# Kernel optimization log

Hardware: AMD Instinct MI355X
Metric: run time of the kernel (lower is better)

## Reference

```python
import jax, jax.numpy as jnp
import numpy as np

B, L, T, IN, H, OUT = 1024, 64, 128, 13, 64, 13
NEG = -1e30


def gru_step(x, h, Wih, Whh, bih, bhh):
    # PyTorch GRU cell: gates ordered (r, z, n)
    gi = x @ Wih.T + bih          # [B, 3H]
    gh = h @ Whh.T + bhh          # [B, 3H]
    ir, iz, inn = jnp.split(gi, 3, axis=-1)
    hr, hz, hn = jnp.split(gh, 3, axis=-1)
    r = jax.nn.sigmoid(ir + hr)
    z = jax.nn.sigmoid(iz + hz)
    n = jnp.tanh(inn + r * hn)
    return (1.0 - z) * n + z * h


def setup_inputs() -> dict:
    key = jax.random.key(0)
    ks = jax.random.split(key, 10)
    s = float(1.0 / np.sqrt(H))
    x = jax.random.normal(ks[0], (B, L, IN), jnp.float32)
    lengths = jax.random.randint(ks[1], (B,), 1, L + 1).at[0].set(L)
    Wih = jax.random.uniform(ks[2], (3 * H, IN), jnp.float32, -s, s)
    Whh = jax.random.uniform(ks[3], (3 * H, H), jnp.float32, -s, s)
    bih = jax.random.uniform(ks[4], (3 * H,), jnp.float32, -s, s)
    bhh = jax.random.uniform(ks[5], (3 * H,), jnp.float32, -s, s)
    Wf = jax.random.uniform(ks[6], (OUT, H), jnp.float32, -s, s)
    bf = jax.random.uniform(ks[7], (OUT,), jnp.float32, -s, s)
    Wa = jax.random.uniform(ks[8], (H, H), jnp.float32, -s, s)
    ba = jax.random.uniform(ks[9], (H,), jnp.float32, -s, s)
    return dict(x=x, lengths=lengths, output_length=T, Wih=Wih, Whh=Whh,
                bih=bih, bhh=bhh, Wf=Wf, bf=bf, Wa=Wa, ba=ba)


def reference(x, lengths, output_length, Wih, Whh, bih, bhh, Wf, bf, Wa, ba):
    b, l = x.shape[0], x.shape[1]
    xT = jnp.swapaxes(x, 0, 1)                        # [L, B, IN]
    h0 = jnp.zeros((b, H), x.dtype)

    # Encoder: masked GRU emulating pack_padded/pad_packed semantics:
    # hidden frozen past each sequence's length; outputs zero past length.
    def enc(h, inp):
        t, xt = inp
        hn = gru_step(xt, h, Wih, Whh, bih, bhh)
        valid = (t < lengths)[:, None]
        h = jnp.where(valid, hn, h)
        return h, jnp.where(valid, hn, 0.0)

    h, outs = jax.lax.scan(enc, h0, (jnp.arange(l), xT))
    # output[:, -1, :] of the padded output (zeros for seqs shorter than max)
    nin = outs[-1] @ Wf.T + bf                        # [B, OUT]

    Tn = output_length
    buf0 = jnp.zeros((Tn, b, H), x.dtype)             # growing past-prediction buffer

    def dec(carry, t):
        h, buf, nin = carry
        hn = gru_step(nin, h, Wih, Whh, bih, bhh)     # output_lstm == hidden (1 layer, 1 step)
        # attention recomputed over all past predictions (softmax over time axis)
        logits = jnp.einsum('tbh,gh->tbg', buf, Wa) + ba      # [T, B, H]
        logits = jnp.where((jnp.arange(Tn) < t)[:, None, None], logits, NEG)
        w = jax.nn.softmax(logits, axis=0)
        o = hn + jnp.sum(w * buf, axis=0)             # at t=0 buffer is all zeros -> +0
        y = o @ Wf.T + bf
        return (hn, buf.at[t].set(o), y), y

    _, ys = jax.lax.scan(dec, (h, buf0, nin), jnp.arange(Tn))
    return jnp.swapaxes(ys, 0, 1)                     # [B, T, OUT]
```

## Files before the change

kernel.cpp:

```cpp
#include <hip/hip_runtime.h>
#include <stdint.h>
#include <math.h>

#define BATCH 1024
#define SEQL  64
#define TDEC  128
#define NIN   13
#define NH    64
#define NOUT  13

typedef _Float16 h2 __attribute__((ext_vector_type(2)));
typedef __fp16   g2 __attribute__((ext_vector_type(2)));

union FU  { uint32_t u; float f; };
union HU  { uint16_t u; _Float16 h; };
union H2U { uint32_t u; h2 h; g2 g; };

__device__ __forceinline__ float bf2f(uint16_t v) { FU t; t.u = ((uint32_t)v) << 16; return t.f; }
__device__ __forceinline__ float hf2f(uint16_t v) { HU t; t.u = v; return (float)t.h; }

__device__ __forceinline__ float ldf(const void* p, long i, int mode) {
    if (mode == 1) return bf2f(((const uint16_t*)p)[i]);
    if (mode == 2) return hf2f(((const uint16_t*)p)[i]);
    return ((const float*)p)[i];
}

__device__ __forceinline__ bool pass_stats(const void* p, int n, int lane, int mode,
                                           float band_lo, float band_hi, float max_ok) {
    int m = (n + 1) / 2;
    int cnt = (m < 64) ? m : 64;
    bool ok_max = true, in_band = false;
    if (lane < cnt) {
        long pos = 2L * (((long)lane * m) / cnt);
        float v = (mode == 1) ? bf2f(((const uint16_t*)p)[pos])
                              : hf2f(((const uint16_t*)p)[pos]);
        float a = fabsf(v);
        ok_max  = (a <= max_ok);
        in_band = (a >= band_lo && a <= band_hi);
    }
    bool allmax = __all(ok_max);
    int nb = (int)__popcll(__ballot(in_band));
    int need = cnt / 4; if (need < 1) need = 1;
    return allmax && (nb >= need);
}
__device__ __forceinline__ int detect(const void* p, int n, int lane,
                                      float band_lo, float band_hi, float max_ok) {
    if (pass_stats(p, n, lane, 1, band_lo, band_hi, max_ok)) return 1;
    if (pass_stats(p, n, lane, 2, band_lo, band_hi, max_ok)) return 2;
    return 0;
}
__device__ __forceinline__ bool detect_len64(const int* p, int lane) {
    int v = p[2 * lane + 1];
    return __all(v == 0);
}

__device__ __forceinline__ float dot2(h2 a, h2 b, float c) {
#if __has_builtin(__builtin_amdgcn_fdot2)
    return __builtin_amdgcn_fdot2(a, b, c, false);
#else
    return c + (float)a[0] * (float)b[0] + (float)a[1] * (float)b[1];
#endif
}
__device__ __forceinline__ uint32_t pku(float a, float b) {
    H2U t; t.g = __builtin_amdgcn_cvt_pkrtz(a, b); return t.u;
}
__device__ __forceinline__ h2 uh(uint32_t u) { H2U t; t.u = u; return t.h; }
__device__ __forceinline__ float rcp_(float x) { return __builtin_amdgcn_rcpf(x); }
__device__ __forceinline__ float sigm(float x)  { return rcp_(1.0f + __expf(-x)); }
__device__ __forceinline__ float tanh_(float x) { return 1.0f - 2.0f * rcp_(__expf(2.0f * x) + 1.0f); }
__device__ __forceinline__ void wb() { __builtin_amdgcn_wave_barrier(); }

__device__ __forceinline__ float swap1(float v) {
    FU a; a.f = v;
    FU b; b.u = (uint32_t)__builtin_amdgcn_mov_dpp((int)a.u, 0xB1, 0xF, 0xF, true);
    return b.f;
}

#define BCAST32(vreg, dst)                                                 \
    {                                                                      \
        uint32_t _pr = pku((vreg), swap1(vreg));                           \
        _Pragma("unroll")                                                  \
        for (int _k = 0; _k < 32; ++_k)                                    \
            (dst)[_k] = __builtin_amdgcn_readlane(_pr, 2 * _k);            \
    }

__global__ __launch_bounds__(64, 1)
void gru_attn_kernel(const void* __restrict__ x, const int* __restrict__ lengths,
                     const void* __restrict__ Wih, const void* __restrict__ Whh,
                     const void* __restrict__ bih, const void* __restrict__ bhh,
                     const void* __restrict__ Wf, const void* __restrict__ bfv,
                     const void* __restrict__ Wa, const void* __restrict__ ba,
                     float* __restrict__ out)
{
    const int b = blockIdx.x;
    const int j = threadIdx.x;

    __shared__ __align__(16) uint32_t xs2[SEQL][8];

    const int dX   = detect(x,   BATCH * SEQL * NIN, j, 0.25f, 4.0f, 16.0f);
    const int dWih = detect(Wih, 3 * NH * NIN, j, 0.04f, 0.13f, 0.14f);
    const int dWhh = detect(Whh, 3 * NH * NH,  j, 0.04f, 0.13f, 0.14f);
    const int dBih = detect(bih, 3 * NH,       j, 0.04f, 0.13f, 0.14f);
    const int dBhh = detect(bhh, 3 * NH,       j, 0.04f, 0.13f, 0.14f);
    const int dWf  = detect(Wf,  NOUT * NH,    j, 0.04f, 0.13f, 0.14f);
    const int dBf  = detect(bfv, NOUT,         j, 0.04f, 0.13f, 0.14f);
    const int dWa  = detect(Wa,  NH * NH,      j, 0.04f, 0.13f, 0.14f);
    const int dBa  = detect(ba,  NH,           j, 0.04f, 0.13f, 0.14f);
    const bool len64 = detect_len64(lengths, j);

    h2 wihr[7], wihz[7], wihn[7];
    h2 whhr[32], whhz[32], whhn[32];
    h2 wap[32], wfp[32];

#pragma unroll
    for (int k = 0; k < 7; ++k) {
        float a0 = ldf(Wih, (0 * NH + j) * NIN + 2 * k, dWih);
        float a1 = (2 * k + 1 < NIN) ? ldf(Wih, (0 * NH + j) * NIN + 2 * k + 1, dWih) : 0.0f;
        wihr[k] = uh(pku(a0, a1));
        float b0 = ldf(Wih, (1 * NH + j) * NIN + 2 * k, dWih);
        float b1 = (2 * k + 1 < NIN) ? ldf(Wih, (1 * NH + j) * NIN + 2 * k + 1, dWih) : 0.0f;
        wihz[k] = uh(pku(b0, b1));
        float c0 = ldf(Wih, (2 * NH + j) * NIN + 2 * k, dWih);
        float c1 = (2 * k + 1 < NIN) ? ldf(Wih, (2 * NH + j) * NIN + 2 * k + 1, dWih) : 0.0f;
        wihn[k] = uh(pku(c0, c1));
    }
    const int jf = (j < NOUT) ? j : 0;
#pragma unroll
    for (int k = 0; k < 32; ++k) {
        whhr[k] = uh(pku(ldf(Whh, (0 * NH + j) * NH + 2 * k, dWhh),
                         ldf(Whh, (0 * NH + j) * NH + 2 * k + 1, dWhh)));
        whhz[k] = uh(pku(ldf(Whh, (1 * NH + j) * NH + 2 * k, dWhh),
                         ldf(Whh, (1 * NH + j) * NH + 2 * k + 1, dWhh)));
        whhn[k] = uh(pku(ldf(Whh, (2 * NH + j) * NH + 2 * k, dWhh),
                         ldf(Whh, (2 * NH + j) * NH + 2 * k + 1, dWhh)));
        wap[k]  = uh(pku(ldf(Wa, j * NH + 2 * k, dWa),
                         ldf(Wa, j * NH + 2 * k + 1, dWa)));
        wfp[k]  = uh(pku(ldf(Wf, jf * NH + 2 * k, dWf),
                         ldf(Wf, jf * NH + 2 * k + 1, dWf)));
    }

    const float bcr = ldf(bih, j, dBih)          + ldf(bhh, j, dBhh);
    const float bcz = ldf(bih, NH + j, dBih)     + ldf(bhh, NH + j, dBhh);
    const float bni = ldf(bih, 2 * NH + j, dBih);
    const float bnh = ldf(bhh, 2 * NH + j, dBhh);
    const float baj = ldf(ba, j, dBa);
    const float bfj = ldf(bfv, jf, dBf);
    const int len = len64 ? lengths[2 * b] : lengths[b];

    {
        const long base = ((long)b * SEQL + j) * NIN;
        float v[14];
#pragma unroll
        for (int k = 0; k < NIN; ++k) v[k] = ldf(x, base + k, dX);
        v[13] = 0.0f;
#pragma unroll
        for (int p = 0; p < 7; ++p) xs2[j][p] = pku(v[2 * p], v[2 * p + 1]);
        xs2[j][7] = 0u;
    }
    wb();

    float h = 0.0f;
    float out_last = 0.0f;

    uint32_t hpk[32];
    BCAST32(h, hpk);

#pragma unroll 1
    for (int t = 0; t < SEQL; ++t) {
        uint4 q0 = *(const uint4*)xs2[t];
        uint4 q1 = *(const uint4*)(xs2[t] + 4);

        float arA = bcr, azA = bcz, hnA = bnh, anA = bni;
        float arB = 0.0f, azB = 0.0f, hnB = 0.0f;
        float arC = 0.0f, azC = 0.0f, hnC = 0.0f;
        float arD = 0.0f, azD = 0.0f, hnD = 0.0f;
#pragma unroll
        for (int k = 0; k < 32; k += 4) {
            h2 h0 = uh(hpk[k]), h1 = uh(hpk[k + 1]), h2v = uh(hpk[k + 2]), h3 = uh(hpk[k + 3]);
            arA = dot2(whhr[k],     h0, arA); azA = dot2(whhz[k],     h0, azA); hnA = dot2(whhn[k],     h0, hnA);
            arB = dot2(whhr[k + 1], h1, arB); azB = dot2(whhz[k + 1], h1, azB); hnB = dot2(whhn[k + 1], h1, hnB);
            arC = dot2(whhr[k + 2], h2v, arC); azC = dot2(whhz[k + 2], h2v, azC); hnC = dot2(whhn[k + 2], h2v, hnC);
            arD = dot2(whhr[k + 3], h3, arD); azD = dot2(whhz[k + 3], h3, azD); hnD = dot2(whhn[k + 3], h3, hnD);
        }
        {
            uint32_t xw[8] = {q0.x, q0.y, q0.z, q0.w, q1.x, q1.y, q1.z, q1.w};
#pragma unroll
            for (int p = 0; p < 7; ++p) {
                h2 xv = uh(xw[p]);
                arB = dot2(wihr[p], xv, arB);
                azB = dot2(wihz[p], xv, azB);
                anA = dot2(wihn[p], xv, anA);
            }
        }
        float ar = (arA + arB) + (arC + arD);
        float az = (azA + azB) + (azC + azD);
        float hna = (hnA + hnB) + (hnC + hnD);
        float r = sigm(ar);
        float z = sigm(az);
        float n = tanh_(anA + r * hna);
        float hnew = n + z * (h - n);
        if (t < len) h = hnew;
        if (t == SEQL - 1) out_last = (t < len) ? hnew : 0.0f;
        BCAST32(h, hpk);
    }

    uint32_t ypk[7];
    {
        uint32_t opk[32];
        BCAST32(out_last, opk);
        float nA = bfj, nB = 0.0f, nC = 0.0f, nD = 0.0f;
#pragma unroll
        for (int k = 0; k < 32; k += 4) {
            nA = dot2(wfp[k],     uh(opk[k]),     nA);
            nB = dot2(wfp[k + 1], uh(opk[k + 1]), nB);
            nC = dot2(wfp[k + 2], uh(opk[k + 2]), nC);
            nD = dot2(wfp[k + 3], uh(opk[k + 3]), nD);
        }
        float nv = (nA + nB) + (nC + nD);
        float nz = (j < NOUT) ? nv : 0.0f;
        uint32_t pr = pku(nz, swap1(nz));
#pragma unroll
        for (int k = 0; k < 7; ++k) ypk[k] = __builtin_amdgcn_readlane(pr, 2 * k);
    }

    float m = -1e30f, Zs = 0.0f, num = 0.0f;

#pragma unroll 1
    for (int t = 0; t < TDEC; ++t) {
        float arA = bcr, azA = bcz, hnA = bnh, anA = bni;
        float arB = 0.0f, azB = 0.0f, hnB = 0.0f;
        float arC = 0.0f, azC = 0.0f, hnC = 0.0f;
        float arD = 0.0f, azD = 0.0f, hnD = 0.0f;
#pragma unroll
        for (int k = 0; k < 32; k += 4) {
            h2 h0 = uh(hpk[k]), h1 = uh(hpk[k + 1]), h2v = uh(hpk[k + 2]), h3 = uh(hpk[k + 3]);
            arA = dot2(whhr[k],     h0, arA); azA = dot2(whhz[k],     h0, azA); hnA = dot2(whhn[k],     h0, hnA);
            arB = dot2(whhr[k + 1], h1, arB); azB = dot2(whhz[k + 1], h1, azB); hnB = dot2(whhn[k + 1], h1, hnB);
            arC = dot2(whhr[k + 2], h2v, arC); azC = dot2(whhz[k + 2], h2v, azC); hnC = dot2(whhn[k + 2], h2v, hnC);
            arD = dot2(whhr[k + 3], h3, arD); azD = dot2(whhz[k + 3], h3, azD); hnD = dot2(whhn[k + 3], h3, hnD);
        }
#pragma unroll
        for (int p = 0; p < 7; ++p) {
            h2 xv = uh(ypk[p]);
            arB = dot2(wihr[p], xv, arB);
            azB = dot2(wihz[p], xv, azB);
            anA = dot2(wihn[p], xv, anA);
        }
        float ar = (arA + arB) + (arC + arD);
        float az = (azA + azB) + (azC + azD);
        float hna = (hnA + hnB) + (hnC + hnD);
        float r = sigm(ar);
        float z = sigm(az);
        float n = tanh_(anA + r * hna);
        float hnew = n + z * (h - n);
        h = hnew;
        float attn = (t > 0) ? num * rcp_(Zs) : 0.0f;
        float o = hnew + attn;

        BCAST32(hnew, hpk);
        uint32_t opk[32];
        BCAST32(o, opk);

        float sA = baj, yA = bfj, sB = 0.0f, yB = 0.0f, sC = 0.0f, yC = 0.0f, sD = 0.0f, yD = 0.0f;
#pragma unroll
        for (int k = 0; k < 32; k += 4) {
            h2 o0 = uh(opk[k]), o1 = uh(opk[k + 1]), o2 = uh(opk[k + 2]), o3 = uh(opk[k + 3]);
            sA = dot2(wap[k],     o0, sA); yA = dot2(wfp[k],     o0, yA);
            sB = dot2(wap[k + 1], o1, sB); yB = dot2(wfp[k + 1], o1, yB);
            sC = dot2(wap[k + 2], o2, sC); yC = dot2(wfp[k + 2], o2, yC);
            sD = dot2(wap[k + 3], o3, sD); yD = dot2(wfp[k + 3], o3, yD);
        }
        float s  = (sA + sB) + (sC + sD);
        float yv = (yA + yB) + (yC + yD);
        float mn = fmaxf(m, s);
        float al = __expf(m - mn);
        float p  = __expf(s - mn);
        Zs  = Zs * al + p;
        num = num * al + p * o;
        m = mn;
        if (j < NOUT) out[((size_t)b * TDEC + t) * NOUT + j] = yv;
        float yz = (j < NOUT) ? yv : 0.0f;
        uint32_t pr = pku(yz, swap1(yz));
#pragma unroll
        for (int k = 0; k < 7; ++k) ypk[k] = __builtin_amdgcn_readlane(pr, 2 * k);
    }
}

extern "C" void kernel_launch(void* const* d_in, const int* in_sizes, int n_in,
                              void* d_out, int out_size, void* d_ws, size_t ws_size,
                              hipStream_t stream) {
    (void)in_sizes; (void)n_in; (void)out_size; (void)d_ws; (void)ws_size;
    const void* x      = d_in[0];
    const int* lengths = (const int*)d_in[1];
    const void* Wih = d_in[3];
    const void* Whh = d_in[4];
    const void* bih = d_in[5];
    const void* bhh = d_in[6];
    const void* Wf  = d_in[7];
    const void* bf  = d_in[8];
    const void* Wa  = d_in[9];
    const void* ba  = d_in[10];
    float* out = (float*)d_out;

    gru_attn_kernel<<<dim3(BATCH), dim3(64), 0, stream>>>(
        x, lengths, Wih, Whh, bih, bhh, Wf, bf, Wa, ba, out);
}
```

Measured before the change: 224.3 us.

## Batch 16 sequences per wave and compute GRU and attention with MFMA

```diff
diff --git a/kernel.cpp b/kernel.cpp
--- a/kernel.cpp
+++ b/kernel.cpp
@@ -8,13 +8,17 @@
 #define NIN   13
 #define NH    64
 #define NOUT  13
-
-typedef _Float16 h2 __attribute__((ext_vector_type(2)));
-typedef __fp16   g2 __attribute__((ext_vector_type(2)));
+#define NB    16
+
+typedef float    f32x4 __attribute__((ext_vector_type(4)));
+typedef _Float16 f16x8 __attribute__((ext_vector_type(8)));
+typedef _Float16 h2    __attribute__((ext_vector_type(2)));
+typedef __fp16   g2    __attribute__((ext_vector_type(2)));
 
 union FU  { uint32_t u; float f; };
 union HU  { uint16_t u; _Float16 h; };
 union H2U { uint32_t u; h2 h; g2 g; };
+union FRG { uint32_t u[4]; f16x8 v; };
 
 __device__ __forceinline__ float bf2f(uint16_t v) { FU t; t.u = ((uint32_t)v) << 16; return t.f; }
 __device__ __forceinline__ float hf2f(uint16_t v) { HU t; t.u = v; return (float)t.h; }
@@ -54,34 +58,93 @@
     return __all(v == 0);
 }
 
-__device__ __forceinline__ float dot2(h2 a, h2 b, float c) {
-#if __has_builtin(__builtin_amdgcn_fdot2)
-    return __builtin_amdgcn_fdot2(a, b, c, false);
-#else
-    return c + (float)a[0] * (float)b[0] + (float)a[1] * (float)b[1];
-#endif
-}
 __device__ __forceinline__ uint32_t pku(float a, float b) {
     H2U t; t.g = __builtin_amdgcn_cvt_pkrtz(a, b); return t.u;
 }
-__device__ __forceinline__ h2 uh(uint32_t u) { H2U t; t.u = u; return t.h; }
 __device__ __forceinline__ float rcp_(float x) { return __builtin_amdgcn_rcpf(x); }
-__device__ __forceinline__ float sigm(float x)  { return rcp_(1.0f + __expf(-x)); }
-__device__ __forceinline__ float tanh_(float x) { return 1.0f - 2.0f * rcp_(__expf(2.0f * x) + 1.0f); }
-__device__ __forceinline__ void wb() { __builtin_amdgcn_wave_barrier(); }
-
-__device__ __forceinline__ float swap1(float v) {
-    FU a; a.f = v;
-    FU b; b.u = (uint32_t)__builtin_amdgcn_mov_dpp((int)a.u, 0xB1, 0xF, 0xF, true);
-    return b.f;
-}
-
-#define BCAST32(vreg, dst)                                                 \
+__device__ __forceinline__ float exp2_(float x) {
+#if __has_builtin(__builtin_amdgcn_exp2f)
+    return __builtin_amdgcn_exp2f(x);
+#else
+    return __expf(x * 0.69314718056f);
+#endif
+}
+__device__ __forceinline__ float sigm2(float xs)  { return rcp_(1.0f + exp2_(-xs)); }
+__device__ __forceinline__ float tanh2(float xs)  { return 1.0f - 2.0f * rcp_(exp2_(xs) + 1.0f); }
+
+#define MFMA(A, B, C) __builtin_amdgcn_mfma_f32_16x16x32_f16((A), (B), (C), 0, 0, 0)
+
+
+__device__ __forceinline__ f16x8 afrag_w(const void* W, int dt, int row, int stride,
+                                         int kbase, int g, float scale) {
+    float v[8];
+#pragma unroll
+    for (int jj = 0; jj < 4; ++jj)
+        v[jj] = ldf(W, (long)row * stride + kbase + 4 * g + jj, dt) * scale;
+#pragma unroll
+    for (int jj = 0; jj < 4; ++jj)
+        v[4 + jj] = ldf(W, (long)row * stride + kbase + 16 + 4 * g + jj, dt) * scale;
+    FRG t;
+    t.u[0] = pku(v[0], v[1]); t.u[1] = pku(v[2], v[3]);
+    t.u[2] = pku(v[4], v[5]); t.u[3] = pku(v[6], v[7]);
+    return t.v;
+}
+__device__ __forceinline__ f16x8 afrag_ih(const void* W, int dt, int row, int g,
+                                          float bias, float scale) {
+    float v[4];
+#pragma unroll
+    for (int jj = 0; jj < 4; ++jj) {
+        int k = 4 * g + jj;
+        v[jj] = (k < NIN) ? ldf(W, (long)row * NIN + k, dt) * scale
+                          : ((k == NIN) ? bias * scale : 0.0f);
+    }
+    FRG t;
+    t.u[0] = pku(v[0], v[1]); t.u[1] = pku(v[2], v[3]);
+    t.u[2] = 0u; t.u[3] = 0u;
+    return t.v;
+}
+__device__ __forceinline__ f16x8 afrag_wf(const void* W, int dt, int row16,
+                                          int kbase, int g) {
+    float v[8];
+#pragma unroll
+    for (int jj = 0; jj < 4; ++jj)
+        v[jj] = (row16 < NOUT) ? ldf(W, (long)row16 * NH + kbase + 4 * g + jj, dt) : 0.0f;
+#pragma unroll
+    for (int jj = 0; jj < 4; ++jj)
+        v[4 + jj] = (row16 < NOUT) ? ldf(W, (long)row16 * NH + kbase + 16 + 4 * g + jj, dt) : 0.0f;
+    FRG t;
+    t.u[0] = pku(v[0], v[1]); t.u[1] = pku(v[2], v[3]);
+    t.u[2] = pku(v[4], v[5]); t.u[3] = pku(v[6], v[7]);
+    return t.v;
+}
+
+#define PACKB(S, F0, F1)                                                   \
+    { FRG _a, _b;                                                          \
+      _a.u[0] = pku(S[0][0], S[0][1]); _a.u[1] = pku(S[0][2], S[0][3]);    \
+      _a.u[2] = pku(S[1][0], S[1][1]); _a.u[3] = pku(S[1][2], S[1][3]);    \
+      _b.u[0] = pku(S[2][0], S[2][1]); _b.u[1] = pku(S[2][2], S[2][3]);    \
+      _b.u[2] = pku(S[3][0], S[3][1]); _b.u[3] = pku(S[3][2], S[3][3]);    \
+      (F0) = _a.v; (F1) = _b.v; }
+
+#define GATES(BF)                                                          \
+    f32x4 dR[4], dZ[4], dNh[4], dNi[4];                                    \
     {                                                                      \
-        uint32_t _pr = pku((vreg), swap1(vreg));                           \
-        _Pragma("unroll")                                                  \
-        for (int _k = 0; _k < 32; ++_k)                                    \
-            (dst)[_k] = __builtin_amdgcn_readlane(_pr, 2 * _k);            \
+        f32x4 zz = {0.0f, 0.0f, 0.0f, 0.0f};                               \
+        _Pragma("unroll") for (int mt = 0; mt < 4; ++mt) {                 \
+            dR[mt]  = MFMA(Ar[mt][0], hbF0, zz);                           \
+            dZ[mt]  = MFMA(Az[mt][0], hbF0, zz);                           \
+            dNh[mt] = MFMA(An[mt][0], hbF0, zz);                           \
+        }                                                                  \
+        _Pragma("unroll") for (int mt = 0; mt < 4; ++mt) {                 \
+            dR[mt]  = MFMA(Ar[mt][1], hbF1, dR[mt]);                       \
+            dZ[mt]  = MFMA(Az[mt][1], hbF1, dZ[mt]);                       \
+            dNh[mt] = MFMA(An[mt][1], hbF1, dNh[mt]);                      \
+        }                                                                  \
+        _Pragma("unroll") for (int mt = 0; mt < 4; ++mt) {                 \
+            dR[mt]  = MFMA(Air[mt], BF, dR[mt]);                           \
+            dZ[mt]  = MFMA(Aiz[mt], BF, dZ[mt]);                           \
+            dNi[mt] = MFMA(Ain[mt], BF, zz);                               \
+        }                                                                  \
     }
 
 __global__ __launch_bounds__(64, 1)
@@ -92,197 +155,210 @@
                      const void* __restrict__ Wa, const void* __restrict__ ba,
                      float* __restrict__ out)
 {
-    const int b = blockIdx.x;
-    const int j = threadIdx.x;
-
-    __shared__ __align__(16) uint32_t xs2[SEQL][8];
-
-    const int dX   = detect(x,   BATCH * SEQL * NIN, j, 0.25f, 4.0f, 16.0f);
-    const int dWih = detect(Wih, 3 * NH * NIN, j, 0.04f, 0.13f, 0.14f);
-    const int dWhh = detect(Whh, 3 * NH * NH,  j, 0.04f, 0.13f, 0.14f);
-    const int dBih = detect(bih, 3 * NH,       j, 0.04f, 0.13f, 0.14f);
-    const int dBhh = detect(bhh, 3 * NH,       j, 0.04f, 0.13f, 0.14f);
-    const int dWf  = detect(Wf,  NOUT * NH,    j, 0.04f, 0.13f, 0.14f);
-    const int dBf  = detect(bfv, NOUT,         j, 0.04f, 0.13f, 0.14f);
-    const int dWa  = detect(Wa,  NH * NH,      j, 0.04f, 0.13f, 0.14f);
-    const int dBa  = detect(ba,  NH,           j, 0.04f, 0.13f, 0.14f);
-    const bool len64 = detect_len64(lengths, j);
-
-    h2 wihr[7], wihz[7], wihn[7];
-    h2 whhr[32], whhz[32], whhn[32];
-    h2 wap[32], wfp[32];
-
-#pragma unroll
-    for (int k = 0; k < 7; ++k) {
-        float a0 = ldf(Wih, (0 * NH + j) * NIN + 2 * k, dWih);
-        float a1 = (2 * k + 1 < NIN) ? ldf(Wih, (0 * NH + j) * NIN + 2 * k + 1, dWih) : 0.0f;
-        wihr[k] = uh(pku(a0, a1));
-        float b0 = ldf(Wih, (1 * NH + j) * NIN + 2 * k, dWih);
-        float b1 = (2 * k + 1 < NIN) ? ldf(Wih, (1 * NH + j) * NIN + 2 * k + 1, dWih) : 0.0f;
-        wihz[k] = uh(pku(b0, b1));
-        float c0 = ldf(Wih, (2 * NH + j) * NIN + 2 * k, dWih);
-        float c1 = (2 * k + 1 < NIN) ? ldf(Wih, (2 * NH + j) * NIN + 2 * k + 1, dWih) : 0.0f;
-        wihn[k] = uh(pku(c0, c1));
-    }
-    const int jf = (j < NOUT) ? j : 0;
-#pragma unroll
-    for (int k = 0; k < 32; ++k) {
-        whhr[k] = uh(pku(ldf(Whh, (0 * NH + j) * NH + 2 * k, dWhh),
-                         ldf(Whh, (0 * NH + j) * NH + 2 * k + 1, dWhh)));
-        whhz[k] = uh(pku(ldf(Whh, (1 * NH + j) * NH + 2 * k, dWhh),
-                         ldf(Whh, (1 * NH + j) * NH + 2 * k + 1, dWhh)));
-        whhn[k] = uh(pku(ldf(Whh, (2 * NH + j) * NH + 2 * k, dWhh),
-                         ldf(Whh, (2 * NH + j) * NH + 2 * k + 1, dWhh)));
-        wap[k]  = uh(pku(ldf(Wa, j * NH + 2 * k, dWa),
-                         ldf(Wa, j * NH + 2 * k + 1, dWa)));
-        wfp[k]  = uh(pku(ldf(Wf, jf * NH + 2 * k, dWf),
-                         ldf(Wf, jf * NH + 2 * k + 1, dWf)));
-    }
-
-    const float bcr = ldf(bih, j, dBih)          + ldf(bhh, j, dBhh);
-    const float bcz = ldf(bih, NH + j, dBih)     + ldf(bhh, NH + j, dBhh);
-    const float bni = ldf(bih, 2 * NH + j, dBih);
-    const float bnh = ldf(bhh, 2 * NH + j, dBhh);
-    const float baj = ldf(ba, j, dBa);
-    const float bfj = ldf(bfv, jf, dBf);
-    const int len = len64 ? lengths[2 * b] : lengths[b];
-
+    const int l  = threadIdx.x;
+    const int g  = l >> 4;
+    const int c  = l & 15;
+    const int b0 = blockIdx.x * NB;
+
+    const int dX   = detect(x,   BATCH * SEQL * NIN, l, 0.25f, 4.0f, 16.0f);
+    const int dWih = detect(Wih, 3 * NH * NIN, l, 0.04f, 0.13f, 0.14f);
+    const int dWhh = detect(Whh, 3 * NH * NH,  l, 0.04f, 0.13f, 0.14f);
+    const int dBih = detect(bih, 3 * NH,       l, 0.04f, 0.13f, 0.14f);
+    const int dBhh = detect(bhh, 3 * NH,       l, 0.04f, 0.13f, 0.14f);
+    const int dWf  = detect(Wf,  NOUT * NH,    l, 0.04f, 0.13f, 0.14f);
+    const int dBf  = detect(bfv, NOUT,         l, 0.04f, 0.13f, 0.14f);
+    const int dWa  = detect(Wa,  NH * NH,      l, 0.04f, 0.13f, 0.14f);
+    const int dBa  = detect(ba,  NH,           l, 0.04f, 0.13f, 0.14f);
+    const bool len64 = detect_len64(lengths, l);
+
+    const float L2E  = 1.44269504089f;
+    const float L2E2 = 2.88539008177f;
+
+    f16x8 Ar[4][2], Az[4][2], An[4][2];
+    f16x8 Air[4], Aiz[4], Ain[4];
+    f16x8 Awa[4][2], Awf[2];
+
+#pragma unroll
+    for (int mt = 0; mt < 4; ++mt) {
+#pragma unroll
+        for (int kc = 0; kc < 2; ++kc) {
+            Ar[mt][kc] = afrag_w(Whh, dWhh,       mt * 16 + c, NH, kc * 32, g, L2E);
+            Az[mt][kc] = afrag_w(Whh, dWhh,  64 + mt * 16 + c, NH, kc * 32, g, L2E);
+            An[mt][kc] = afrag_w(Whh, dWhh, 128 + mt * 16 + c, NH, kc * 32, g, L2E2);
+            Awa[mt][kc] = afrag_w(Wa, dWa,        mt * 16 + c, NH, kc * 32, g, L2E);
+        }
+        int rr = mt * 16 + c;
+        float br = ldf(bih, rr, dBih)            + ldf(bhh, rr, dBhh);
+        float bz = ldf(bih, NH + rr, dBih)       + ldf(bhh, NH + rr, dBhh);
+        float bn = ldf(bih, 2 * NH + rr, dBih);
+        Air[mt] = afrag_ih(Wih, dWih,            rr, g, br, L2E);
+        Aiz[mt] = afrag_ih(Wih, dWih,  64 + rr,     g, bz, L2E);
+        Ain[mt] = afrag_ih(Wih, dWih, 128 + rr,     g, bn, L2E2);
+    }
+#pragma unroll
+    for (int kc = 0; kc < 2; ++kc) Awf[kc] = afrag_wf(Wf, dWf, c, kc * 32, g);
+
+    float bnhS[4][4], bajS[4][4], bfS[4];
+#pragma unroll
+    for (int mt = 0; mt < 4; ++mt)
+#pragma unroll
+        for (int reg = 0; reg < 4; ++reg) {
+            int row = mt * 16 + 4 * g + reg;
+            bnhS[mt][reg] = ldf(bhh, 2 * NH + row, dBhh) * L2E2;
+            bajS[mt][reg] = ldf(ba, row, dBa) * L2E;
+        }
+#pragma unroll
+    for (int reg = 0; reg < 4; ++reg) {
+        int row = 4 * g + reg;
+        bfS[reg] = (row < NOUT) ? ldf(bfv, row, dBf) : 0.0f;
+    }
+
+    const int lenc = len64 ? lengths[2 * (b0 + c)] : lengths[b0 + c];
+
+    float hc[4][4];
+    float ol[4][4];
+#pragma unroll
+    for (int mt = 0; mt < 4; ++mt)
+#pragma unroll
+        for (int reg = 0; reg < 4; ++reg) { hc[mt][reg] = 0.0f; ol[mt][reg] = 0.0f; }
+    f16x8 hbF0, hbF1;
+    { FRG zf; zf.u[0] = zf.u[1] = zf.u[2] = zf.u[3] = 0u; hbF0 = zf.v; hbF1 = zf.v; }
+
+    float xpre[4];
     {
-        const long base = ((long)b * SEQL + j) * NIN;
-        float v[14];
-#pragma unroll
-        for (int k = 0; k < NIN; ++k) v[k] = ldf(x, base + k, dX);
-        v[13] = 0.0f;
-#pragma unroll
-        for (int p = 0; p < 7; ++p) xs2[j][p] = pku(v[2 * p], v[2 * p + 1]);
-        xs2[j][7] = 0u;
-    }
-    wb();
-
-    float h = 0.0f;
-    float out_last = 0.0f;
-
-    uint32_t hpk[32];
-    BCAST32(h, hpk);
+        const long base = ((long)(b0 + c) * SEQL + 0) * NIN;
+#pragma unroll
+        for (int jj = 0; jj < 4; ++jj) {
+            int k = 4 * g + jj;
+            xpre[jj] = (k < NIN) ? ldf(x, base + k, dX) : ((k == NIN) ? 1.0f : 0.0f);
+        }
+    }
 
 #pragma unroll 1
     for (int t = 0; t < SEQL; ++t) {
-        uint4 q0 = *(const uint4*)xs2[t];
-        uint4 q1 = *(const uint4*)(xs2[t] + 4);
-
-        float arA = bcr, azA = bcz, hnA = bnh, anA = bni;
-        float arB = 0.0f, azB = 0.0f, hnB = 0.0f;
-        float arC = 0.0f, azC = 0.0f, hnC = 0.0f;
-        float arD = 0.0f, azD = 0.0f, hnD = 0.0f;
-#pragma unroll
-        for (int k = 0; k < 32; k += 4) {
-            h2 h0 = uh(hpk[k]), h1 = uh(hpk[k + 1]), h2v = uh(hpk[k + 2]), h3 = uh(hpk[k + 3]);
-            arA = dot2(whhr[k],     h0, arA); azA = dot2(whhz[k],     h0, azA); hnA = dot2(whhn[k],     h0, hnA);
-            arB = dot2(whhr[k + 1], h1, arB); azB = dot2(whhz[k + 1], h1, azB); hnB = dot2(whhn[k + 1], h1, hnB);
-            arC = dot2(whhr[k + 2], h2v, arC); azC = dot2(whhz[k + 2], h2v, azC); hnC = dot2(whhn[k + 2], h2v, hnC);
-            arD = dot2(whhr[k + 3], h3, arD); azD = dot2(whhz[k + 3], h3, azD); hnD = dot2(whhn[k + 3], h3, hnD);
-        }
+        FRG xb;
+        xb.u[0] = pku(xpre[0], xpre[1]);
+        xb.u[1] = pku(xpre[2], xpre[3]);
+        xb.u[2] = 0u; xb.u[3] = 0u;
+        f16x8 xbF = xb.v;
         {
-            uint32_t xw[8] = {q0.x, q0.y, q0.z, q0.w, q1.x, q1.y, q1.z, q1.w};
-#pragma unroll
-            for (int p = 0; p < 7; ++p) {
-                h2 xv = uh(xw[p]);
-                arB = dot2(wihr[p], xv, arB);
-                azB = dot2(wihz[p], xv, azB);
-                anA = dot2(wihn[p], xv, anA);
-            }
-        }
-        float ar = (arA + arB) + (arC + arD);
-        float az = (azA + azB) + (azC + azD);
-        float hna = (hnA + hnB) + (hnC + hnD);
-        float r = sigm(ar);
-        float z = sigm(az);
-        float n = tanh_(anA + r * hna);
-        float hnew = n + z * (h - n);
-        if (t < len) h = hnew;
-        if (t == SEQL - 1) out_last = (t < len) ? hnew : 0.0f;
-        BCAST32(h, hpk);
-    }
-
-    uint32_t ypk[7];
+            int tt = (t + 1 < SEQL) ? t + 1 : t;
+            const long base = ((long)(b0 + c) * SEQL + tt) * NIN;
+#pragma unroll
+            for (int jj = 0; jj < 4; ++jj) {
+                int k = 4 * g + jj;
+                xpre[jj] = (k < NIN) ? ldf(x, base + k, dX) : ((k == NIN) ? 1.0f : 0.0f);
+            }
+        }
+
+        GATES(xbF)
+
+#pragma unroll
+        for (int mt = 0; mt < 4; ++mt)
+#pragma unroll
+            for (int reg = 0; reg < 4; ++reg) {
+                float rr = sigm2(dR[mt][reg]);
+                float zv = sigm2(dZ[mt][reg]);
+                float nn = tanh2(dNi[mt][reg] + rr * (dNh[mt][reg] + bnhS[mt][reg]));
+                float hn = nn + zv * (hc[mt][reg] - nn);
+                bool upd = (t < lenc);
+                if (t == SEQL - 1) ol[mt][reg] = upd ? hn : 0.0f;
+                hc[mt][reg] = upd ? hn : hc[mt][reg];
+            }
+        PACKB(hc, hbF0, hbF1)
+    }
+
+    f16x8 ybF;
     {
-        uint32_t opk[32];
-        BCAST32(out_last, opk);
-        float nA = bfj, nB = 0.0f, nC = 0.0f, nD = 0.0f;
-#pragma unroll
-        for (int k = 0; k < 32; k += 4) {
-            nA = dot2(wfp[k],     uh(opk[k]),     nA);
-            nB = dot2(wfp[k + 1], uh(opk[k + 1]), nB);
-            nC = dot2(wfp[k + 2], uh(opk[k + 2]), nC);
-            nD = dot2(wfp[k + 3], uh(opk[k + 3]), nD);
-        }
-        float nv = (nA + nB) + (nC + nD);
-        float nz = (j < NOUT) ? nv : 0.0f;
-        uint32_t pr = pku(nz, swap1(nz));
-#pragma unroll
-        for (int k = 0; k < 7; ++k) ypk[k] = __builtin_amdgcn_readlane(pr, 2 * k);
-    }
-
-    float m = -1e30f, Zs = 0.0f, num = 0.0f;
+        f16x8 obF0, obF1;
+        PACKB(ol, obF0, obF1)
+        f32x4 zz = {0.0f, 0.0f, 0.0f, 0.0f};
+        f32x4 dY = MFMA(Awf[0], obF0, zz);
+        dY = MFMA(Awf[1], obF1, dY);
+        float yv[4];
+#pragma unroll
+        for (int reg = 0; reg < 4; ++reg) yv[reg] = dY[reg] + bfS[reg];
+        float y1 = (g == 3) ? 1.0f : yv[1];
+        FRG yb;
+        yb.u[0] = pku(yv[0], y1);
+        yb.u[1] = pku(yv[2], yv[3]);
+        yb.u[2] = 0u; yb.u[3] = 0u;
+        ybF = yb.v;
+    }
+
+    float mS[4][4], ZS[4][4], numS[4][4];
+#pragma unroll
+    for (int mt = 0; mt < 4; ++mt)
+#pragma unroll
+        for (int reg = 0; reg < 4; ++reg) {
+            mS[mt][reg] = -1e30f; ZS[mt][reg] = 0.0f; numS[mt][reg] = 0.0f;
+        }
 
 #pragma unroll 1
     for (int t = 0; t < TDEC; ++t) {
-        float arA = bcr, azA = bcz, hnA = bnh, anA = bni;
-        float arB = 0.0f, azB = 0.0f, hnB = 0.0f;
-        float arC = 0.0f, azC = 0.0f, hnC = 0.0f;
-        float arD = 0.0f, azD = 0.0f, hnD = 0.0f;
-#pragma unroll
-        for (int k = 0; k < 32; k += 4) {
-            h2 h0 = uh(hpk[k]), h1 = uh(hpk[k + 1]), h2v = uh(hpk[k + 2]), h3 = uh(hpk[k + 3]);
-            arA = dot2(whhr[k],     h0, arA); azA = dot2(whhz[k],     h0, azA); hnA = dot2(whhn[k],     h0, hnA);
-            arB = dot2(whhr[k + 1], h1, arB); azB = dot2(whhz[k + 1], h1, azB); hnB = dot2(whhn[k + 1], h1, hnB);
-            arC = dot2(whhr[k + 2], h2v, arC); azC = dot2(whhz[k + 2], h2v, azC); hnC = dot2(whhn[k + 2], h2v, hnC);
-            arD = dot2(whhr[k + 3], h3, arD); azD = dot2(whhz[k + 3], h3, azD); hnD = dot2(whhn[k + 3], h3, hnD);
-        }
-#pragma unroll
-        for (int p = 0; p < 7; ++p) {
-            h2 xv = uh(ypk[p]);
-            arB = dot2(wihr[p], xv, arB);
-            azB = dot2(wihz[p], xv, azB);
-            anA = dot2(wihn[p], xv, anA);
-        }
-        float ar = (arA + arB) + (arC + arD);
-        float az = (azA + azB) + (azC + azD);
-        float hna = (hnA + hnB) + (hnC + hnD);
-        float r = sigm(ar);
-        float z = sigm(az);
-        float n = tanh_(anA + r * hna);
-        float hnew = n + z * (h - n);
-        h = hnew;
-        float attn = (t > 0) ? num * rcp_(Zs) : 0.0f;
-        float o = hnew + attn;
-
-        BCAST32(hnew, hpk);
-        uint32_t opk[32];
-        BCAST32(o, opk);
-
-        float sA = baj, yA = bfj, sB = 0.0f, yB = 0.0f, sC = 0.0f, yC = 0.0f, sD = 0.0f, yD = 0.0f;
-#pragma unroll
-        for (int k = 0; k < 32; k += 4) {
-            h2 o0 = uh(opk[k]), o1 = uh(opk[k + 1]), o2 = uh(opk[k + 2]), o3 = uh(opk[k + 3]);
-            sA = dot2(wap[k],     o0, sA); yA = dot2(wfp[k],     o0, yA);
-            sB = dot2(wap[k + 1], o1, sB); yB = dot2(wfp[k + 1], o1, yB);
-            sC = dot2(wap[k + 2], o2, sC); yC = dot2(wfp[k + 2], o2, yC);
-            sD = dot2(wap[k + 3], o3, sD); yD = dot2(wfp[k + 3], o3, yD);
-        }
-        float s  = (sA + sB) + (sC + sD);
-        float yv = (yA + yB) + (yC + yD);
-        float mn = fmaxf(m, s);
-        float al = __expf(m - mn);
-        float p  = __expf(s - mn);
-        Zs  = Zs * al + p;
-        num = num * al + p * o;
-        m = mn;
-        if (j < NOUT) out[((size_t)b * TDEC + t) * NOUT + j] = yv;
-        float yz = (j < NOUT) ? yv : 0.0f;
-        uint32_t pr = pku(yz, swap1(yz));
-#pragma unroll
-        for (int k = 0; k < 7; ++k) ypk[k] = __builtin_amdgcn_readlane(pr, 2 * k);
+        GATES(ybF)
+
+#pragma unroll
+        for (int mt = 0; mt < 4; ++mt)
+#pragma unroll
+            for (int reg = 0; reg < 4; ++reg) {
+                float rr = sigm2(dR[mt][reg]);
+                float zv = sigm2(dZ[mt][reg]);
+                float nn = tanh2(dNi[mt][reg] + rr * (dNh[mt][reg] + bnhS[mt][reg]));
+                hc[mt][reg] = nn + zv * (hc[mt][reg] - nn);
+            }
+        PACKB(hc, hbF0, hbF1)
+
+        float oc[4][4];
+#pragma unroll
+        for (int mt = 0; mt < 4; ++mt)
+#pragma unroll
+            for (int reg = 0; reg < 4; ++reg) {
+                float a_ = numS[mt][reg] * rcp_(ZS[mt][reg]);
+                oc[mt][reg] = hc[mt][reg] + ((t > 0) ? a_ : 0.0f);
+            }
+        f16x8 obF0, obF1;
+        PACKB(oc, obF0, obF1)
+
+        f32x4 dS[4], dY;
+        {
+            f32x4 zz = {0.0f, 0.0f, 0.0f, 0.0f};
+#pragma unroll
+            for (int mt = 0; mt < 4; ++mt) dS[mt] = MFMA(Awa[mt][0], obF0, zz);
+#pragma unroll
+            for (int mt = 0; mt < 4; ++mt) dS[mt] = MFMA(Awa[mt][1], obF1, dS[mt]);
+            dY = MFMA(Awf[0], obF0, zz);
+            dY = MFMA(Awf[1], obF1, dY);
+        }
+
+#pragma unroll
+        for (int mt = 0; mt < 4; ++mt)
+#pragma unroll
+            for (int reg = 0; reg < 4; ++reg) {
+                float s_ = dS[mt][reg] + bajS[mt][reg];
+                float mn = fmaxf(mS[mt][reg], s_);
+                float al = exp2_(mS[mt][reg] - mn);
+                float pp = exp2_(s_ - mn);
+                ZS[mt][reg]  = ZS[mt][reg] * al + pp;
+                numS[mt][reg] = numS[mt][reg] * al + pp * oc[mt][reg];
+                mS[mt][reg] = mn;
+            }
+
+        float yv[4];
+#pragma unroll
+        for (int reg = 0; reg < 4; ++reg) yv[reg] = dY[reg] + bfS[reg];
+#pragma unroll
+        for (int reg = 0; reg < 4; ++reg) {
+            int row = 4 * g + reg;
+            if (row < NOUT)
+                out[((size_t)(b0 + c) * TDEC + t) * NOUT + row] = yv[reg];
+        }
+        float y1 = (g == 3) ? 1.0f : yv[1];
+        FRG yb;
+        yb.u[0] = pku(yv[0], y1);
+        yb.u[1] = pku(yv[2], yv[3]);
+        yb.u[2] = 0u; yb.u[3] = 0u;
+        ybF = yb.v;
     }
 }
 
@@ -302,6 +378,6 @@
     const void* ba  = d_in[10];
     float* out = (float*)d_out;
 
-    gru_attn_kernel<<<dim3(BATCH), dim3(64), 0, stream>>>(
+    gru_attn_kernel<<<dim3(BATCH / NB), dim3(64), 0, stream>>>(
         x, lengths, Wih, Whh, bih, bhh, Wf, bf, Wa, ba, out);
 }
```

After: 472.8 us. 111% more time.
